# Kernel tuning notes

Measured on AMD Instinct MI355X. Metric: run time of the kernel, lower is better.

The kernel has to match this reference:

```python
import jax, jax.numpy as jnp
import numpy as np

N_NODES = 100000
N_EDGES = 1250000
D_IN, D_HID, D_OUT = 64, 64, 64


def _sage_conv(x, edge_index, W_l, b_l, W_r, num_nodes):
    # PyG SAGEConv (aggr='mean', root_weight=True):
    #   out_i = W_l @ mean_{j->i} x_j + b_l + W_r @ x_i
    src, dst = edge_index[0], edge_index[1]
    msgs = x[src]  # [E, D] gather
    agg = jax.ops.segment_sum(msgs, dst, num_segments=num_nodes)  # [N, D]
    cnt = jax.ops.segment_sum(jnp.ones((src.shape[0],), x.dtype), dst,
                              num_segments=num_nodes)
    mean = agg / jnp.maximum(cnt, 1.0)[:, None]
    return mean @ W_l.T + b_l + x @ W_r.T


def setup_inputs() -> dict:
    key = jax.random.key(0)
    ks = jax.random.split(key, 8)
    s_in = 1.0 / np.sqrt(D_IN)
    s_hid = 1.0 / np.sqrt(D_HID)
    return {
        "x": jax.random.normal(ks[0], (N_NODES, D_IN), jnp.float32),
        "edge_index": jax.random.randint(ks[1], (2, N_EDGES), 0, N_NODES, jnp.int32),
        "W1_l": jax.random.normal(ks[2], (D_HID, D_IN), jnp.float32) * s_in,
        "b1": jnp.zeros((D_HID,), jnp.float32),
        "W1_r": jax.random.normal(ks[3], (D_HID, D_IN), jnp.float32) * s_in,
        "W2_l": jax.random.normal(ks[4], (D_OUT, D_HID), jnp.float32) * s_hid,
        "b2": jnp.zeros((D_OUT,), jnp.float32),
        "W2_r": jax.random.normal(ks[5], (D_OUT, D_HID), jnp.float32) * s_hid,
    }


def reference(x, edge_index, W1_l, b1, W1_r, W2_l, b2, W2_r):
    n = x.shape[0]
    h = _sage_conv(x, edge_index, W1_l, b1, W1_r, n)
    h = jax.nn.relu(h)
    # F.dropout(p=0.1, training=self.training): identity in eval mode
    out = _sage_conv(h, edge_index, W2_l, b2, W2_r, n)
    return out
```

## Files before the change

kernel.cpp:

```cpp
#include <hip/hip_runtime.h>

#define D 64
#define CAP 4096
#define CHUNK 4096
#define MROW_STRIDE 72

typedef unsigned int u32;
typedef unsigned short u16;
typedef __attribute__((ext_vector_type(8))) short bf16x8_t;
typedef __attribute__((ext_vector_type(4))) float f32x4_t;

__device__ __forceinline__ u16 f2b(float f) {
  u32 u = __float_as_uint(f);
  u += 0x7FFFu + ((u >> 16) & 1u);
  return (u16)(u >> 16);
}
__device__ __forceinline__ float hi2f(u32 u) { return __uint_as_float(u & 0xFFFF0000u); }
__device__ __forceinline__ float lo2f(u32 u) { return __uint_as_float(u << 16); }

__launch_bounds__(256)
__global__ void k_cast(const float* __restrict__ x, u16* __restrict__ xb, int total8) {
  int i = blockIdx.x * 256 + threadIdx.x;
  int stride = gridDim.x * 256;
  for (; i < total8; i += stride) {
    const float4* p = (const float4*)(x + (size_t)i * 8);
    float4 v0 = p[0], v1 = p[1];
    uint4 w;
    w.x = (u32)f2b(v0.x) | ((u32)f2b(v0.y) << 16);
    w.y = (u32)f2b(v0.z) | ((u32)f2b(v0.w) << 16);
    w.z = (u32)f2b(v1.x) | ((u32)f2b(v1.y) << 16);
    w.w = (u32)f2b(v1.z) | ((u32)f2b(v1.w) << 16);
    *(uint4*)(xb + (size_t)i * 8) = w;
  }
}

__launch_bounds__(512)
__global__ void k_prep(const float* __restrict__ W1l, const float* __restrict__ W1r,
                       const float* __restrict__ W2l, const float* __restrict__ W2r,
                       u16* __restrict__ Bp1, u16* __restrict__ Bp2,
                       int* __restrict__ bcur, int* __restrict__ rowptr,
                       int n, int nE, int nb) {
  int t = threadIdx.x;
  if (blockIdx.x == 2) {
    if (t < nb) bcur[t] = t * CAP;
    if (t == 0) rowptr[n] = nE;
    return;
  }
  const float* Wl = blockIdx.x ? W2l : W1l;
  const float* Wr = blockIdx.x ? W2r : W1r;
  u16* Bp = blockIdx.x ? Bp2 : Bp1;
  for (int idx = t; idx < 8192; idx += 512) {
    int j = idx & 7;
    int lane = (idx >> 3) & 63;
    int st = idx >> 9;
    int s = st >> 2, tt = st & 3;
    int k = s * 32 + ((lane >> 4) << 3) + j;
    int c = tt * 16 + (lane & 15);
    float v = (k < 64) ? Wl[c * 64 + k] : Wr[c * 64 + (k - 64)];
    Bp[idx] = f2b(v);
  }
}

__launch_bounds__(512)
__global__ void k_bin(const int* __restrict__ src, const int* __restrict__ dst,
                      int* __restrict__ bcur, u32* __restrict__ ebuf, int nE, int nb) {
  __shared__ int hist[512];
  __shared__ int excl[512];
  __shared__ int lcur[512];
  __shared__ int gstart[512];
  __shared__ u32 ent[CHUNK];
  __shared__ u16 ebkt[CHUNK];

  int t = threadIdx.x;
  int base = blockIdx.x * CHUNK;
  int cnt = nE - base; if (cnt > CHUNK) cnt = CHUNK;

  hist[t] = 0;
  __syncthreads();

  int ls[8], ld[8];
  #pragma unroll
  for (int k = 0; k < 8; ++k) {
    int i = t + k * 512;
    if (i < cnt) {
      ls[k] = src[base + i];
      ld[k] = dst[base + i];
      atomicAdd(&hist[ld[k] >> 8], 1);
    } else ls[k] = -1;
  }
  __syncthreads();

  int bcnt = hist[t];
  for (int off = 1; off < 512; off <<= 1) {
    int u = (t >= off) ? hist[t - off] : 0;
    __syncthreads();
    hist[t] += u;
    __syncthreads();
  }
  int ex = hist[t] - bcnt;
  excl[t] = ex;
  lcur[t] = ex;
  if (t < nb && bcnt > 0) gstart[t] = atomicAdd(&bcur[t], bcnt);
  __syncthreads();

  #pragma unroll
  for (int k = 0; k < 8; ++k) {
    if (ls[k] >= 0) {
      int b = ld[k] >> 8;
      int p = atomicAdd(&lcur[b], 1);
      ent[p]  = ((u32)ls[k] << 8) | (u32)(ld[k] & 255);
      ebkt[p] = (u16)b;
    }
  }
  __syncthreads();

  for (int i = t; i < cnt; i += 512) {
    int b = ebkt[i];
    ebuf[gstart[b] + (i - excl[b])] = ent[i];
  }
}

__launch_bounds__(256)
__global__ void k_build(const u32* __restrict__ ebuf, const int* __restrict__ bcur,
                        int* __restrict__ rowptr, int* __restrict__ csr, int n) {
  __shared__ int hist[256];
  __shared__ int lcur[256];
  __shared__ int sbase;
  int b = blockIdx.x;
  int t = threadIdx.x;
  int base_s = b * CAP;
  int cnt = bcur[b] - base_s;

  int ps = 0;
  for (int i = t; i < b; i += 256) ps += bcur[i] - i * CAP;
  hist[t] = ps;
  __syncthreads();
  for (int off = 128; off > 0; off >>= 1) {
    if (t < off) hist[t] += hist[t + off];
    __syncthreads();
  }
  if (t == 0) sbase = hist[0];
  __syncthreads();
  int base_d = sbase;

  hist[t] = 0;
  __syncthreads();
  for (int i = t; i < cnt; i += 256)
    atomicAdd(&hist[ebuf[base_s + i] & 255], 1);
  __syncthreads();

  int v = hist[t];
  for (int off = 1; off < 256; off <<= 1) {
    int u = (t >= off) ? hist[t - off] : 0;
    __syncthreads();
    hist[t] += u;
    __syncthreads();
  }
  int ex = hist[t] - v;
  int node = b * 256 + t;
  if (node < n) rowptr[node] = base_d + ex;
  lcur[t] = ex;
  __syncthreads();

  for (int i = t; i < cnt; i += 256) {
    u32 e = ebuf[base_s + i];
    int p = atomicAdd(&lcur[e & 255], 1);
    csr[base_d + p] = (int)(e >> 8);
  }
}

__launch_bounds__(256)
__global__ void k_gd(const int* __restrict__ rowptr, const int* __restrict__ csr,
                     const u16* __restrict__ xin, const u16* __restrict__ Bp,
                     const float* __restrict__ bias,
                     u16* __restrict__ out_bf, float* __restrict__ out_f32,
                     int n, int do_relu) {
  __shared__ int idx_s[4][4][64];
  __shared__ u16 mrow[16 * MROW_STRIDE];

  int wave = threadIdx.x >> 6;
  int lane = threadIdx.x & 63;
  int g = lane >> 4;
  int q = lane & 15;
  int node0 = blockIdx.x * 16;
  int local = wave * 4 + g;
  int node = node0 + local;

  int rs = rowptr[node];
  int re = rowptr[node + 1];

  float a0 = 0.f, a1 = 0.f, a2 = 0.f, a3 = 0.f;
  for (int cb = rs; cb < re; cb += 64) {
    int mcnt = re - cb; if (mcnt > 64) mcnt = 64;
    #pragma unroll
    for (int k = 0; k < 4; ++k) {
      int sidx = k * 16 + q;
      if (sidx < mcnt) idx_s[wave][g][sidx] = csr[cb + sidx];
    }
    int j = 0;
    for (; j + 4 <= mcnt; j += 4) {
      int i0 = idx_s[wave][g][j];
      int i1 = idx_s[wave][g][j + 1];
      int i2 = idx_s[wave][g][j + 2];
      int i3 = idx_s[wave][g][j + 3];
      uint2 v0 = *(const uint2*)(xin + (size_t)i0 * D + q * 4);
      uint2 v1 = *(const uint2*)(xin + (size_t)i1 * D + q * 4);
      uint2 v2 = *(const uint2*)(xin + (size_t)i2 * D + q * 4);
      uint2 v3 = *(const uint2*)(xin + (size_t)i3 * D + q * 4);
      a0 += lo2f(v0.x); a1 += hi2f(v0.x); a2 += lo2f(v0.y); a3 += hi2f(v0.y);
      a0 += lo2f(v1.x); a1 += hi2f(v1.x); a2 += lo2f(v1.y); a3 += hi2f(v1.y);
      a0 += lo2f(v2.x); a1 += hi2f(v2.x); a2 += lo2f(v2.y); a3 += hi2f(v2.y);
      a0 += lo2f(v3.x); a1 += hi2f(v3.x); a2 += lo2f(v3.y); a3 += hi2f(v3.y);
    }
    for (; j < mcnt; ++j) {
      int i0 = idx_s[wave][g][j];
      uint2 v0 = *(const uint2*)(xin + (size_t)i0 * D + q * 4);
      a0 += lo2f(v0.x); a1 += hi2f(v0.x); a2 += lo2f(v0.y); a3 += hi2f(v0.y);
    }
  }

  float inv = 1.0f / fmaxf((float)(re - rs), 1.0f);
  uint2 w;
  w.x = (u32)f2b(a0 * inv) | ((u32)f2b(a1 * inv) << 16);
  w.y = (u32)f2b(a2 * inv) | ((u32)f2b(a3 * inv) << 16);
  *(uint2*)(mrow + local * MROW_STRIDE + q * 4) = w;
  __syncthreads();

  const bf16x8_t* Bp8 = (const bf16x8_t*)Bp;
  int arow = node0 + (lane & 15);
  const bf16x8_t* xr8 = (const bf16x8_t*)(xin + (size_t)arow * D);
  int ko = lane >> 4;

  f32x4_t acc = {};
  #pragma unroll
  for (int s = 0; s < 4; ++s) {
    bf16x8_t a;
    if (s < 2) a = *(const bf16x8_t*)(mrow + (lane & 15) * MROW_STRIDE + s * 32 + ko * 8);
    else       a = xr8[(s - 2) * 4 + ko];
    bf16x8_t b = Bp8[(s * 4 + wave) * 64 + lane];
    acc = __builtin_amdgcn_mfma_f32_16x16x32_bf16(a, b, acc, 0, 0, 0);
  }

  int f = wave * 16 + (lane & 15);
  float bv = bias[f];
  int r0 = (lane >> 4) * 4;
  #pragma unroll
  for (int r = 0; r < 4; ++r) {
    int row = node0 + r0 + r;
    float v = acc[r] + bv;
    if (do_relu) v = fmaxf(v, 0.f);
    if (out_bf) out_bf[(size_t)row * D + f] = f2b(v);
    else        out_f32[(size_t)row * D + f] = v;
  }
}

extern "C" void kernel_launch(void* const* d_in, const int* in_sizes, int n_in,
                              void* d_out, int out_size, void* d_ws, size_t ws_size,
                              hipStream_t stream) {
  const float* x   = (const float*)d_in[0];
  const int*   ei  = (const int*)d_in[1];
  const float* W1l = (const float*)d_in[2];
  const float* b1  = (const float*)d_in[3];
  const float* W1r = (const float*)d_in[4];
  const float* W2l = (const float*)d_in[5];
  const float* b2  = (const float*)d_in[6];
  const float* W2r = (const float*)d_in[7];

  int n  = in_sizes[0] / D;
  int nE = in_sizes[1] / 2;
  const int* src = ei;
  const int* dst = ei + nE;
  int nb = (n + 255) / 256;

  char* w = (char*)d_ws;
  auto alloc = [&](size_t bytes) { char* p = w; w += (bytes + 255) & ~(size_t)255; return p; };
  int* bcur   = (int*)alloc((size_t)nb * 4);
  int* rowptr = (int*)alloc((size_t)(n + 1) * 4);
  int* csr    = (int*)alloc((size_t)nE * 4);
  u16* xb     = (u16*)alloc((size_t)n * D * 2);
  size_t hbytes = (size_t)n * D * 2;
  size_t ebytes = (size_t)nb * CAP * 4;
  char* hov   = alloc(hbytes > ebytes ? hbytes : ebytes);
  u32* ebuf   = (u32*)hov;
  u16* hb     = (u16*)hov;
  u16* Bp1    = (u16*)alloc(8192 * 2);
  u16* Bp2    = (u16*)alloc(8192 * 2);

  int eblocks = (nE + CHUNK - 1) / CHUNK;
  int gdblocks = n / 16;

  k_cast  <<<2048,    256, 0, stream>>>(x, xb, n * D / 8);
  k_prep  <<<3,       512, 0, stream>>>(W1l, W1r, W2l, W2r, Bp1, Bp2,
                                        bcur, rowptr, n, nE, nb);
  k_bin   <<<eblocks, 512, 0, stream>>>(src, dst, bcur, ebuf, nE, nb);
  k_build <<<nb,      256, 0, stream>>>(ebuf, bcur, rowptr, csr, n);

  k_gd<<<gdblocks, 256, 0, stream>>>(rowptr, csr, xb, Bp1, b1, hb, nullptr, n, 1);
  k_gd<<<gdblocks, 256, 0, stream>>>(rowptr, csr, hb, Bp2, b2, nullptr, (float*)d_out, n, 0);
}
```

Measured before the change: 109.7 us.

## Sort nodes by in-degree for balanced gather blocks and merge prep kernels

Computes a per-bucket in-degree histogram in k_build and a new k_perm kernel builds a permutation that groups nodes in descending degree order. The gather kernels process 16 nodes per block through this permutation, so waves in a block see similar edge counts and less lane/wave imbalance. It also folds the weight-packing and counter-init kernel into the cast kernel to drop one launch. The cost is an extra kernel, extra histogram traffic, and scattered (non-contiguous) row reads and writes in the MFMA stage.

```diff
diff --git a/kernel.cpp b/kernel.cpp
--- a/kernel.cpp
+++ b/kernel.cpp
@@ -19,45 +19,42 @@
 __device__ __forceinline__ float lo2f(u32 u) { return __uint_as_float(u << 16); }
 
 __launch_bounds__(256)
-__global__ void k_cast(const float* __restrict__ x, u16* __restrict__ xb, int total8) {
-  int i = blockIdx.x * 256 + threadIdx.x;
-  int stride = gridDim.x * 256;
-  for (; i < total8; i += stride) {
-    const float4* p = (const float4*)(x + (size_t)i * 8);
-    float4 v0 = p[0], v1 = p[1];
-    uint4 w;
-    w.x = (u32)f2b(v0.x) | ((u32)f2b(v0.y) << 16);
-    w.y = (u32)f2b(v0.z) | ((u32)f2b(v0.w) << 16);
-    w.z = (u32)f2b(v1.x) | ((u32)f2b(v1.y) << 16);
-    w.w = (u32)f2b(v1.z) | ((u32)f2b(v1.w) << 16);
-    *(uint4*)(xb + (size_t)i * 8) = w;
-  }
-}
-
-__launch_bounds__(512)
-__global__ void k_prep(const float* __restrict__ W1l, const float* __restrict__ W1r,
+__global__ void k_cast(const float* __restrict__ x, u16* __restrict__ xb, int total8,
+                       const float* __restrict__ W1l, const float* __restrict__ W1r,
                        const float* __restrict__ W2l, const float* __restrict__ W2r,
                        u16* __restrict__ Bp1, u16* __restrict__ Bp2,
                        int* __restrict__ bcur, int* __restrict__ rowptr,
                        int n, int nE, int nb) {
+  int b = blockIdx.x;
   int t = threadIdx.x;
-  if (blockIdx.x == 2) {
-    if (t < nb) bcur[t] = t * CAP;
+  if (b < 2048) {
+    for (int i = b * 256 + t; i < total8; i += 2048 * 256) {
+      const float4* p = (const float4*)(x + (size_t)i * 8);
+      float4 v0 = p[0], v1 = p[1];
+      uint4 w;
+      w.x = (u32)f2b(v0.x) | ((u32)f2b(v0.y) << 16);
+      w.y = (u32)f2b(v0.z) | ((u32)f2b(v0.w) << 16);
+      w.z = (u32)f2b(v1.x) | ((u32)f2b(v1.y) << 16);
+      w.w = (u32)f2b(v1.z) | ((u32)f2b(v1.w) << 16);
+      *(uint4*)(xb + (size_t)i * 8) = w;
+    }
+  } else if (b < 2050) {
+    const float* Wl = (b == 2049) ? W2l : W1l;
+    const float* Wr = (b == 2049) ? W2r : W1r;
+    u16* Bp = (b == 2049) ? Bp2 : Bp1;
+    for (int idx = t; idx < 8192; idx += 256) {
+      int j = idx & 7;
+      int lane = (idx >> 3) & 63;
+      int st = idx >> 9;
+      int s = st >> 2, tt = st & 3;
+      int k = s * 32 + ((lane >> 4) << 3) + j;
+      int c = tt * 16 + (lane & 15);
+      float v = (k < 64) ? Wl[c * 64 + k] : Wr[c * 64 + (k - 64)];
+      Bp[idx] = f2b(v);
+    }
+  } else {
+    for (int i = t; i < nb; i += 256) bcur[i] = i * CAP;
     if (t == 0) rowptr[n] = nE;
-    return;
-  }
-  const float* Wl = blockIdx.x ? W2l : W1l;
-  const float* Wr = blockIdx.x ? W2r : W1r;
-  u16* Bp = blockIdx.x ? Bp2 : Bp1;
-  for (int idx = t; idx < 8192; idx += 512) {
-    int j = idx & 7;
-    int lane = (idx >> 3) & 63;
-    int st = idx >> 9;
-    int s = st >> 2, tt = st & 3;
-    int k = s * 32 + ((lane >> 4) << 3) + j;
-    int c = tt * 16 + (lane & 15);
-    float v = (k < 64) ? Wl[c * 64 + k] : Wr[c * 64 + (k - 64)];
-    Bp[idx] = f2b(v);
   }
 }
 
@@ -122,15 +119,19 @@
 
 __launch_bounds__(256)
 __global__ void k_build(const u32* __restrict__ ebuf, const int* __restrict__ bcur,
-                        int* __restrict__ rowptr, int* __restrict__ csr, int n) {
+                        int* __restrict__ rowptr, int* __restrict__ csr,
+                        int* __restrict__ bh, int n, int nbB) {
   __shared__ int hist[256];
   __shared__ int lcur[256];
+  __shared__ int dh[64];
   __shared__ int sbase;
   int b = blockIdx.x;
   int t = threadIdx.x;
   int base_s = b * CAP;
   int cnt = bcur[b] - base_s;
 
+  if (t < 64) dh[t] = 0;
+
   int ps = 0;
   for (int i = t; i < b; i += 256) ps += bcur[i] - i * CAP;
   hist[t] = ps;
@@ -150,6 +151,9 @@
   __syncthreads();
 
   int v = hist[t];
+  int node = b * 256 + t;
+  if (node < n) atomicAdd(&dh[v > 63 ? 63 : v], 1);
+
   for (int off = 1; off < 256; off <<= 1) {
     int u = (t >= off) ? hist[t - off] : 0;
     __syncthreads();
@@ -157,10 +161,11 @@
     __syncthreads();
   }
   int ex = hist[t] - v;
-  int node = b * 256 + t;
   if (node < n) rowptr[node] = base_d + ex;
   lcur[t] = ex;
   __syncthreads();
+
+  if (t < 64) bh[t * nbB + b] = dh[t];
 
   for (int i = t; i < cnt; i += 256) {
     u32 e = ebuf[base_s + i];
@@ -170,21 +175,56 @@
 }
 
 __launch_bounds__(256)
+__global__ void k_perm(const int* __restrict__ rowptr, const int* __restrict__ bh,
+                       int* __restrict__ perm, int n, int nbB) {
+  __shared__ int rowoff[64], total[64], colbase[64], cur[64];
+  int t = threadIdx.x, b = blockIdx.x;
+  if (t < 64) {
+    int ro = 0, tot = 0;
+    const int* row = bh + t * nbB;
+    for (int i = 0; i < nbB; ++i) {
+      int c = row[i];
+      if (i < b) ro += c;
+      tot += c;
+    }
+    rowoff[t] = ro; total[t] = tot; cur[t] = 0;
+  }
+  __syncthreads();
+  if (t == 0) {
+    int s = 0;
+    for (int d = 63; d >= 0; --d) { colbase[d] = s; s += total[d]; }
+  }
+  __syncthreads();
+  int node = b * 256 + t;
+  if (node < n) {
+    int d = rowptr[node + 1] - rowptr[node]; if (d > 63) d = 63;
+    int r = atomicAdd(&cur[d], 1);
+    perm[colbase[d] + rowoff[d] + r] = node;
+  }
+}
+
+__launch_bounds__(256)
 __global__ void k_gd(const int* __restrict__ rowptr, const int* __restrict__ csr,
+                     const int* __restrict__ perm,
                      const u16* __restrict__ xin, const u16* __restrict__ Bp,
                      const float* __restrict__ bias,
                      u16* __restrict__ out_bf, float* __restrict__ out_f32,
                      int n, int do_relu) {
   __shared__ int idx_s[4][4][64];
   __shared__ u16 mrow[16 * MROW_STRIDE];
-
-  int wave = threadIdx.x >> 6;
-  int lane = threadIdx.x & 63;
+  __shared__ int perm_s[16];
+
+  int tid = threadIdx.x;
+  int wave = tid >> 6;
+  int lane = tid & 63;
   int g = lane >> 4;
   int q = lane & 15;
   int node0 = blockIdx.x * 16;
   int local = wave * 4 + g;
-  int node = node0 + local;
+
+  if (tid < 16) perm_s[tid] = perm[node0 + tid];
+  __syncthreads();
+  int node = perm_s[local];
 
   int rs = rowptr[node];
   int re = rowptr[node + 1];
@@ -227,7 +267,7 @@
   __syncthreads();
 
   const bf16x8_t* Bp8 = (const bf16x8_t*)Bp;
-  int arow = node0 + (lane & 15);
+  int arow = perm_s[lane & 15];
   const bf16x8_t* xr8 = (const bf16x8_t*)(xin + (size_t)arow * D);
   int ko = lane >> 4;
 
@@ -246,7 +286,7 @@
   int r0 = (lane >> 4) * 4;
   #pragma unroll
   for (int r = 0; r < 4; ++r) {
-    int row = node0 + r0 + r;
+    int row = perm_s[r0 + r];
     float v = acc[r] + bv;
     if (do_relu) v = fmaxf(v, 0.f);
     if (out_bf) out_bf[(size_t)row * D + f] = f2b(v);
@@ -277,6 +317,8 @@
   int* bcur   = (int*)alloc((size_t)nb * 4);
   int* rowptr = (int*)alloc((size_t)(n + 1) * 4);
   int* csr    = (int*)alloc((size_t)nE * 4);
+  int* bh     = (int*)alloc((size_t)64 * nb * 4);
+  int* perm   = (int*)alloc((size_t)n * 4);
   u16* xb     = (u16*)alloc((size_t)n * D * 2);
   size_t hbytes = (size_t)n * D * 2;
   size_t ebytes = (size_t)nb * CAP * 4;
@@ -289,12 +331,12 @@
   int eblocks = (nE + CHUNK - 1) / CHUNK;
   int gdblocks = n / 16;
 
-  k_cast  <<<2048,    256, 0, stream>>>(x, xb, n * D / 8);
-  k_prep  <<<3,       512, 0, stream>>>(W1l, W1r, W2l, W2r, Bp1, Bp2,
-                                        bcur, rowptr, n, nE, nb);
-  k_bin   <<<eblocks, 512, 0, stream>>>(src, dst, bcur, ebuf, nE, nb);
-  k_build <<<nb,      256, 0, stream>>>(ebuf, bcur, rowptr, csr, n);
-
-  k_gd<<<gdblocks, 256, 0, stream>>>(rowptr, csr, xb, Bp1, b1, hb, nullptr, n, 1);
-  k_gd<<<gdblocks, 256, 0, stream>>>(rowptr, csr, hb, Bp2, b2, nullptr, (float*)d_out, n, 0);
-}
+  k_cast <<<2051,    256, 0, stream>>>(x, xb, n * D / 8, W1l, W1r, W2l, W2r,
+                                       Bp1, Bp2, bcur, rowptr, n, nE, nb);
+  k_bin  <<<eblocks, 512, 0, stream>>>(src, dst, bcur, ebuf, nE, nb);
+  k_build<<<nb,      256, 0, stream>>>(ebuf, bcur, rowptr, csr, bh, n, nb);
+  k_perm <<<nb,      256, 0, stream>>>(rowptr, bh, perm, n, nb);
+
+  k_gd<<<gdblocks, 256, 0, stream>>>(rowptr, csr, perm, xb, Bp1, b1, hb, nullptr, n, 1);
+  k_gd<<<gdblocks, 256, 0, stream>>>(rowptr, csr, perm, hb, Bp2, b2, nullptr, (float*)d_out, n, 0);
+}
```

After: 161.9 us. 47.6% more time.
